# Performance work log

Hardware: AMD Instinct MI355X
Metric: run time of the kernel (lower is better)

Reference implementation:

```python
import jax, jax.numpy as jnp
import numpy as np

NEIGHBOR_NUM = 32  # init kwarg neighbor_num

B, N, C = 64, 512, 1024

def setup_inputs() -> dict:
    key = jax.random.key(0)
    x = jax.random.normal(key, (B, N, C), dtype=jnp.float32)
    return {"x": x}

def reference(x):
    # si = x @ x^T (detached in the original -> stop_gradient)
    si = jax.lax.stop_gradient(x)
    si = jnp.einsum('bic,bjc->bij', si, si)  # (b, n, n)
    # k-th largest value per row as threshold
    topv, _ = jax.lax.top_k(si, NEIGHBOR_NUM)          # (b, n, k)
    threshold = topv[..., -1:]                          # (b, n, 1)
    adj = (si >= threshold).astype(si.dtype)            # (b, n, n)
    # normalize_digraph: D^{-1/2} A D^{-1/2} with D = row-degree diag
    node_degrees = adj.sum(axis=-1)                     # (b, n)
    degs_inv_sqrt = node_degrees ** (-0.5)              # (b, n)
    # diag(d) @ A @ diag(d) == d_i * A_ij * d_j
    norm_A = degs_inv_sqrt[:, :, None] * adj * degs_inv_sqrt[:, None, :]
    return norm_A
```

## Files before the change

### kernel.cpp

```cpp
#include <hip/hip_runtime.h>
#include <hip/hip_bf16.h>
#include <math.h>

#define B 64
#define N 512
#define C 1024
#define K_NEIGH 32
#define DELTA 0.625f
#define BISECT_ITERS 14

typedef __attribute__((ext_vector_type(8))) _Float16 half8;
typedef __attribute__((ext_vector_type(4))) float f32x4;

__global__ __launch_bounds__(256) void gemm_f16(const float* __restrict__ x,
                                                float* __restrict__ S) {
    __shared__ half8 Ah[512], Bh[512];

    const int b = blockIdx.x;
    int p = blockIdx.y;
    int ti = 0;
    while (p >= (4 - ti)) { p -= (4 - ti); ti++; }
    const int tj = ti + p;
    const int row0A = ti * 128;
    const int row0B = tj * 128;
    const float* xb = x + (size_t)b * N * C;

    const int t    = threadIdx.x;
    const int w    = t >> 6;
    const int lane = t & 63;
    const int quad = lane >> 4;
    const int lid  = lane & 15;
    const int wr   = (w >> 1) * 64;
    const int wc   = (w & 1) * 64;

    const int srow = t >> 1;
    const int sg   = (t & 1) * 2;

    f32x4 acc[4][4];
#pragma unroll
    for (int r = 0; r < 4; r++)
#pragma unroll
        for (int c = 0; c < 4; c++)
#pragma unroll
            for (int e = 0; e < 4; e++) acc[r][c][e] = 0.f;

    for (int kt = 0; kt < C; kt += 32) {
        {
            const float* pa = xb + (size_t)(row0A + srow) * C + kt + sg * 8;
            float4 f0 = ((const float4*)pa)[0];
            float4 f1 = ((const float4*)pa)[1];
            float4 f2 = ((const float4*)pa)[2];
            float4 f3 = ((const float4*)pa)[3];
            half8 g0, g1;
            g0[0] = (_Float16)f0.x; g0[1] = (_Float16)f0.y; g0[2] = (_Float16)f0.z; g0[3] = (_Float16)f0.w;
            g0[4] = (_Float16)f1.x; g0[5] = (_Float16)f1.y; g0[6] = (_Float16)f1.z; g0[7] = (_Float16)f1.w;
            g1[0] = (_Float16)f2.x; g1[1] = (_Float16)f2.y; g1[2] = (_Float16)f2.z; g1[3] = (_Float16)f2.w;
            g1[4] = (_Float16)f3.x; g1[5] = (_Float16)f3.y; g1[6] = (_Float16)f3.z; g1[7] = (_Float16)f3.w;
            Ah[sg * 128 + srow]       = g0;
            Ah[(sg + 1) * 128 + srow] = g1;
        }
        {
            const float* pb = xb + (size_t)(row0B + srow) * C + kt + sg * 8;
            float4 f0 = ((const float4*)pb)[0];
            float4 f1 = ((const float4*)pb)[1];
            float4 f2 = ((const float4*)pb)[2];
            float4 f3 = ((const float4*)pb)[3];
            half8 g0, g1;
            g0[0] = (_Float16)f0.x; g0[1] = (_Float16)f0.y; g0[2] = (_Float16)f0.z; g0[3] = (_Float16)f0.w;
            g0[4] = (_Float16)f1.x; g0[5] = (_Float16)f1.y; g0[6] = (_Float16)f1.z; g0[7] = (_Float16)f1.w;
            g1[0] = (_Float16)f2.x; g1[1] = (_Float16)f2.y; g1[2] = (_Float16)f2.z; g1[3] = (_Float16)f2.w;
            g1[4] = (_Float16)f3.x; g1[5] = (_Float16)f3.y; g1[6] = (_Float16)f3.z; g1[7] = (_Float16)f3.w;
            Bh[sg * 128 + srow]       = g0;
            Bh[(sg + 1) * 128 + srow] = g1;
        }
        __syncthreads();

        half8 vb[4];
#pragma unroll
        for (int c = 0; c < 4; c++) vb[c] = Bh[quad * 128 + wc + c * 16 + lid];
#pragma unroll
        for (int r = 0; r < 4; r++) {
            half8 va = Ah[quad * 128 + wr + r * 16 + lid];
#pragma unroll
            for (int c = 0; c < 4; c++)
                acc[r][c] = __builtin_amdgcn_mfma_f32_16x16x32_f16(va, vb[c], acc[r][c], 0, 0, 0);
        }
        __syncthreads();
    }

    float* Sb = S + (size_t)b * N * N;
#pragma unroll
    for (int r = 0; r < 4; r++) {
#pragma unroll
        for (int c = 0; c < 4; c++) {
#pragma unroll
            for (int e = 0; e < 4; e++) {
                const int grow = row0A + wr + r * 16 + quad * 4 + e;
                const int gcol = row0B + wc + c * 16 + lid;
                const float vv = acc[r][c][e];
                Sb[(size_t)grow * N + gcol] = vv;
                if (ti != tj) Sb[(size_t)gcol * N + grow] = vv;
            }
        }
    }
}

__global__ __launch_bounds__(256) void thresh_mask(const float* __restrict__ S,
                                                   const float* __restrict__ x,
                                                   unsigned long long* __restrict__ masks,
                                                   float* __restrict__ dinv) {
    const int row  = blockIdx.x * 4 + (threadIdx.x >> 6);
    const int lane = threadIdx.x & 63;
    const float* Srow = S + (size_t)row * N;

    float v0[8];
#pragma unroll
    for (int k = 0; k < 8; k++) v0[k] = Srow[lane + 64 * k];

    float lo = -1400.f, hi = 1400.f;
    for (int it = 0; it < BISECT_ITERS; it++) {
        const float mid = 0.5f * (lo + hi);
        int c = 0;
#pragma unroll
        for (int k = 0; k < 8; k++) c += __popcll(__ballot(v0[k] > mid));
        if (c >= K_NEIGH) lo = mid; else hi = mid;
    }
    const float P   = 0.5f * (lo + hi);
    const float hiB = P + DELTA, loB = P - DELTA;

    int cA = 0;
#pragma unroll
    for (int k = 0; k < 8; k++) cA += __popcll(__ballot(v0[k] > hiB));
    const int m_need = K_NEIGH - cA;

    int cnt = 0, myj = -1;
#pragma unroll
    for (int kq = 0; kq < 8; kq++) {
        unsigned long long bm = __ballot(v0[kq] >= loB && v0[kq] <= hiB);
        while (bm) {
            int bl = __ffsll(bm) - 1;
            bm &= bm - 1;
            if (cnt == lane) myj = bl + 64 * kq;
            cnt++;
        }
    }
    const int nc = cnt < 64 ? cnt : 64;

    const int bb_ = row >> 9, ii = row & (N - 1);
    const float* xi = x + ((size_t)bb_ * N + ii) * C;
    float4 ai[4];
#pragma unroll
    for (int q = 0; q < 4; q++) ai[q] = *(const float4*)(xi + q * 256 + lane * 4);

    float ex = -INFINITY;
    for (int c2 = 0; c2 < nc; c2++) {
        const int j = __shfl(myj, c2);
        const float* xj = x + ((size_t)bb_ * N + j) * C;
        float s = 0.f;
#pragma unroll
        for (int q = 0; q < 4; q++) {
            float4 bv = *(const float4*)(xj + q * 256 + lane * 4);
            s = fmaf(ai[q].x, bv.x, s);
            s = fmaf(ai[q].y, bv.y, s);
            s = fmaf(ai[q].z, bv.z, s);
            s = fmaf(ai[q].w, bv.w, s);
        }
#pragma unroll
        for (int off = 32; off > 0; off >>= 1) s += __shfl_xor(s, off);
        if (lane == c2) ex = s;
    }

    float val = ex, T = -INFINITY;
    for (int it = 0; it < m_need; it++) {
        float M = val;
#pragma unroll
        for (int off = 32; off > 0; off >>= 1) M = fmaxf(M, __shfl_xor(M, off));
        T = M;
        unsigned long long ball = __ballot(val == M);
        int first = __ffsll(ball) - 1;
        if (lane == first) val = -INFINITY;
    }
    const int dec = (lane < nc && ex >= T) ? 1 : 0;

    int bits[8];
#pragma unroll
    for (int kq = 0; kq < 8; kq++) bits[kq] = (v0[kq] > hiB) ? 1 : 0;
    for (int c2 = 0; c2 < nc; c2++) {
        int j = __shfl(myj, c2);
        int d = __shfl(dec, c2);
        if ((j & 63) == lane) bits[j >> 6] = d;
    }

    unsigned long long msk[8];
    int deg = 0;
#pragma unroll
    for (int kq = 0; kq < 8; kq++) {
        msk[kq] = __ballot(bits[kq] != 0);
        deg += __popcll(msk[kq]);
    }
    if (lane == 0) {
#pragma unroll
        for (int kq = 0; kq < 8; kq++) masks[(size_t)row * 8 + kq] = msk[kq];
        dinv[row] = rsqrtf((float)deg);
    }
}

__global__ __launch_bounds__(256) void scale_adj(float* __restrict__ Sout,
                                                 const unsigned long long* __restrict__ masks,
                                                 const float* __restrict__ dinv) {
    const int idx = blockIdx.x * 256 + threadIdx.x;
    const int jq = idx & 127;
    const int i  = (idx >> 7) & (N - 1);
    const int b  = idx >> 16;
    const int row = (b << 9) | i;
    const int j0 = jq * 4;

    const unsigned long long mk = masks[(size_t)row * 8 + (j0 >> 6)];
    const float di = dinv[row];
    float4 dj = ((const float4*)dinv)[(b << 7) | jq];

    float4 o;
    o.x = ((mk >> ((j0 + 0) & 63)) & 1ull) ? di * dj.x : 0.f;
    o.y = ((mk >> ((j0 + 1) & 63)) & 1ull) ? di * dj.y : 0.f;
    o.z = ((mk >> ((j0 + 2) & 63)) & 1ull) ? di * dj.z : 0.f;
    o.w = ((mk >> ((j0 + 3) & 63)) & 1ull) ? di * dj.w : 0.f;
    ((float4*)Sout)[idx] = o;
}

extern "C" void kernel_launch(void* const* d_in, const int* in_sizes, int n_in,
                              void* d_out, int out_size, void* d_ws, size_t ws_size,
                              hipStream_t stream) {
    const float* x = (const float*)d_in[0];
    float* out = (float*)d_out;
    unsigned long long* masks = (unsigned long long*)d_ws;
    float* dinv = (float*)(masks + (size_t)B * N * 8);

    dim3 g1(B, 10);
    gemm_f16<<<g1, 256, 0, stream>>>(x, out);
    thresh_mask<<<B * N / 4, 256, 0, stream>>>(out, x, masks, dinv);
    const int total4 = B * N * N / 4;
    scale_adj<<<total4 / 256, 256, 0, stream>>>(out, masks, dinv);
}
```

Baseline: 329.5 us.

## Compute full tile grid with XCD-aware mapping, deeper K step, diag tile reuse

Replaces the symmetric upper-triangle launch (640 blocks, with transposed uncoalesced stores) by a full 16-tile-per-batch grid (1024 blocks). Each block writes only its own tile, coalesced. Blocks are mapped so that all tiles of one batch land on the same XCD, for L2 reuse of x. The K step doubles to 64, halving barriers, and diagonal tiles skip loading the B operand by reusing A in LDS. The cost is extra MFMA work for the now-redundant lower-triangle tiles, plus larger LDS use per block.

```diff
diff --git a/kernel.cpp b/kernel.cpp
--- a/kernel.cpp
+++ b/kernel.cpp
@@ -12,18 +12,27 @@
 typedef __attribute__((ext_vector_type(8))) _Float16 half8;
 typedef __attribute__((ext_vector_type(4))) float f32x4;
 
-__global__ __launch_bounds__(256) void gemm_f16(const float* __restrict__ x,
-                                                float* __restrict__ S) {
-    __shared__ half8 Ah[512], Bh[512];
-
-    const int b = blockIdx.x;
-    int p = blockIdx.y;
-    int ti = 0;
-    while (p >= (4 - ti)) { p -= (4 - ti); ti++; }
-    const int tj = ti + p;
+__device__ __forceinline__ half8 cvt8(float4 a, float4 b) {
+    half8 g;
+    g[0] = (_Float16)a.x; g[1] = (_Float16)a.y; g[2] = (_Float16)a.z; g[3] = (_Float16)a.w;
+    g[4] = (_Float16)b.x; g[5] = (_Float16)b.y; g[6] = (_Float16)b.z; g[7] = (_Float16)b.w;
+    return g;
+}
+
+__global__ __launch_bounds__(256, 4) void gemm_f16(const float* __restrict__ x,
+                                                   float* __restrict__ S) {
+    __shared__ half8 Ah[1024], Bh[1024];
+
+    const int id   = blockIdx.x;
+    const int xcd  = id & 7;
+    const int slot = id >> 3;
+    const int b    = xcd + 8 * (slot >> 4);
+    const int tile = slot & 15;
+    const int ti = tile >> 2, tj = tile & 3;
     const int row0A = ti * 128;
     const int row0B = tj * 128;
     const float* xb = x + (size_t)b * N * C;
+    const bool diag = (ti == tj);
 
     const int t    = threadIdx.x;
     const int w    = t >> 6;
@@ -34,7 +43,8 @@
     const int wc   = (w & 1) * 64;
 
     const int srow = t >> 1;
-    const int sg   = (t & 1) * 2;
+    const int sgb  = (t & 1) * 4;
+    const int koff = (t & 1) * 32;
 
     f32x4 acc[4][4];
 #pragma unroll
@@ -44,46 +54,41 @@
 #pragma unroll
             for (int e = 0; e < 4; e++) acc[r][c][e] = 0.f;
 
-    for (int kt = 0; kt < C; kt += 32) {
+    for (int kt = 0; kt < C; kt += 64) {
         {
-            const float* pa = xb + (size_t)(row0A + srow) * C + kt + sg * 8;
-            float4 f0 = ((const float4*)pa)[0];
-            float4 f1 = ((const float4*)pa)[1];
-            float4 f2 = ((const float4*)pa)[2];
-            float4 f3 = ((const float4*)pa)[3];
-            half8 g0, g1;
-            g0[0] = (_Float16)f0.x; g0[1] = (_Float16)f0.y; g0[2] = (_Float16)f0.z; g0[3] = (_Float16)f0.w;
-            g0[4] = (_Float16)f1.x; g0[5] = (_Float16)f1.y; g0[6] = (_Float16)f1.z; g0[7] = (_Float16)f1.w;
-            g1[0] = (_Float16)f2.x; g1[1] = (_Float16)f2.y; g1[2] = (_Float16)f2.z; g1[3] = (_Float16)f2.w;
-            g1[4] = (_Float16)f3.x; g1[5] = (_Float16)f3.y; g1[6] = (_Float16)f3.z; g1[7] = (_Float16)f3.w;
-            Ah[sg * 128 + srow]       = g0;
-            Ah[(sg + 1) * 128 + srow] = g1;
-        }
-        {
-            const float* pb = xb + (size_t)(row0B + srow) * C + kt + sg * 8;
-            float4 f0 = ((const float4*)pb)[0];
-            float4 f1 = ((const float4*)pb)[1];
-            float4 f2 = ((const float4*)pb)[2];
-            float4 f3 = ((const float4*)pb)[3];
-            half8 g0, g1;
-            g0[0] = (_Float16)f0.x; g0[1] = (_Float16)f0.y; g0[2] = (_Float16)f0.z; g0[3] = (_Float16)f0.w;
-            g0[4] = (_Float16)f1.x; g0[5] = (_Float16)f1.y; g0[6] = (_Float16)f1.z; g0[7] = (_Float16)f1.w;
-            g1[0] = (_Float16)f2.x; g1[1] = (_Float16)f2.y; g1[2] = (_Float16)f2.z; g1[3] = (_Float16)f2.w;
-            g1[4] = (_Float16)f3.x; g1[5] = (_Float16)f3.y; g1[6] = (_Float16)f3.z; g1[7] = (_Float16)f3.w;
-            Bh[sg * 128 + srow]       = g0;
-            Bh[(sg + 1) * 128 + srow] = g1;
+            const float4* pa = (const float4*)(xb + (size_t)(row0A + srow) * C + kt + koff);
+            float4 f0 = pa[0], f1 = pa[1], f2 = pa[2], f3 = pa[3];
+            float4 f4 = pa[4], f5 = pa[5], f6 = pa[6], f7 = pa[7];
+            Ah[(sgb + 0) * 128 + srow] = cvt8(f0, f1);
+            Ah[(sgb + 1) * 128 + srow] = cvt8(f2, f3);
+            Ah[(sgb + 2) * 128 + srow] = cvt8(f4, f5);
+            Ah[(sgb + 3) * 128 + srow] = cvt8(f6, f7);
+        }
+        if (!diag) {
+            const float4* pb = (const float4*)(xb + (size_t)(row0B + srow) * C + kt + koff);
+            float4 f0 = pb[0], f1 = pb[1], f2 = pb[2], f3 = pb[3];
+            float4 f4 = pb[4], f5 = pb[5], f6 = pb[6], f7 = pb[7];
+            Bh[(sgb + 0) * 128 + srow] = cvt8(f0, f1);
+            Bh[(sgb + 1) * 128 + srow] = cvt8(f2, f3);
+            Bh[(sgb + 2) * 128 + srow] = cvt8(f4, f5);
+            Bh[(sgb + 3) * 128 + srow] = cvt8(f6, f7);
         }
         __syncthreads();
 
-        half8 vb[4];
-#pragma unroll
-        for (int c = 0; c < 4; c++) vb[c] = Bh[quad * 128 + wc + c * 16 + lid];
-#pragma unroll
-        for (int r = 0; r < 4; r++) {
-            half8 va = Ah[quad * 128 + wr + r * 16 + lid];
-#pragma unroll
-            for (int c = 0; c < 4; c++)
-                acc[r][c] = __builtin_amdgcn_mfma_f32_16x16x32_f16(va, vb[c], acc[r][c], 0, 0, 0);
+        const half8* Bs = diag ? Ah : Bh;
+#pragma unroll
+        for (int ks = 0; ks < 2; ks++) {
+            const int so = (ks * 4 + quad) * 128;
+            half8 vb[4];
+#pragma unroll
+            for (int c = 0; c < 4; c++) vb[c] = Bs[so + wc + c * 16 + lid];
+#pragma unroll
+            for (int r = 0; r < 4; r++) {
+                half8 va = Ah[so + wr + r * 16 + lid];
+#pragma unroll
+                for (int c = 0; c < 4; c++)
+                    acc[r][c] = __builtin_amdgcn_mfma_f32_16x16x32_f16(va, vb[c], acc[r][c], 0, 0, 0);
+            }
         }
         __syncthreads();
     }
@@ -97,9 +102,7 @@
             for (int e = 0; e < 4; e++) {
                 const int grow = row0A + wr + r * 16 + quad * 4 + e;
                 const int gcol = row0B + wc + c * 16 + lid;
-                const float vv = acc[r][c][e];
-                Sb[(size_t)grow * N + gcol] = vv;
-                if (ti != tj) Sb[(size_t)gcol * N + grow] = vv;
+                Sb[(size_t)grow * N + gcol] = acc[r][c][e];
             }
         }
     }
@@ -235,8 +238,7 @@
     unsigned long long* masks = (unsigned long long*)d_ws;
     float* dinv = (float*)(masks + (size_t)B * N * 8);
 
-    dim3 g1(B, 10);
-    gemm_f16<<<g1, 256, 0, stream>>>(x, out);
+    gemm_f16<<<dim3(B * 16), 256, 0, stream>>>(x, out);
     thresh_mask<<<B * N / 4, 256, 0, stream>>>(out, x, masks, dinv);
     const int total4 = B * N * N / 4;
     scale_adj<<<total4 / 256, 256, 0, stream>>>(out, masks, dinv);
```

Result: slower. 368.4 us (+11.8%).
